# Kernel optimization log

Measured on AMD Instinct MI355X. Metric: run time of the kernel, lower is better.

Reference implementation:

```python
import jax, jax.numpy as jnp
import numpy as np

VALUE_RANGE = 16
D_MODEL = 1024
NUM_TILES = 8
NUM_FREQS = 6
BATCH = 65536
TEMPERATURE = 0.5


def _fourier(x):
    # x: (B,) -> (B, 2*NUM_FREQS); freqs = 2**[0..F)
    freqs = 2.0 ** jnp.arange(NUM_FREQS, dtype=jnp.float32)
    ang = x[:, None] * (2.0 * np.pi / VALUE_RANGE) * freqs[None, :]
    return jnp.concatenate([jnp.sin(ang), jnp.cos(ang)], axis=-1)


def _layernorm(x, g, b, eps=1e-5):
    m = jnp.mean(x, axis=-1, keepdims=True)
    v = jnp.var(x, axis=-1, keepdims=True)
    return (x - m) * jax.lax.rsqrt(v + eps) * g + b


def _gelu(x):
    return jax.nn.gelu(x, approximate=False)  # torch nn.GELU() default is exact erf


def setup_inputs() -> dict:
    key = jax.random.key(0)
    ks = jax.random.split(key, 16)
    d, T, F4 = D_MODEL, NUM_TILES, 4 * NUM_FREQS
    s = lambda i, shape, scale: (jax.random.normal(ks[i], shape, jnp.float32) * scale)
    return {
        "a": jax.random.uniform(ks[0], (BATCH,), jnp.float32, 0.0, float(VALUE_RANGE)),
        "b": jax.random.uniform(ks[1], (BATCH,), jnp.float32, 0.0, float(VALUE_RANGE)),
        "W_in": s(2, (F4, d), 0.05), "b_in": jnp.zeros((d,), jnp.float32),
        "ln_g": jnp.ones((d,), jnp.float32), "ln_b": jnp.zeros((d,), jnp.float32),
        "Wr1_sum": s(3, (d, d), 0.03), "br1_sum": jnp.zeros((d,), jnp.float32),
        "Wr2_sum": s(4, (d, T), 0.03), "br2_sum": jnp.zeros((T,), jnp.float32),
        "Wr1_diff": s(5, (d, d), 0.03), "br1_diff": jnp.zeros((d,), jnp.float32),
        "Wr2_diff": s(6, (d, T), 0.03), "br2_diff": jnp.zeros((T,), jnp.float32),
        "We1": s(7, (T, d, 2 * d), 0.03), "be1": jnp.zeros((T, 2 * d), jnp.float32),
        "We2": s(8, (T, 2 * d, d), 0.02), "be2": jnp.zeros((T, d), jnp.float32),
        "w_sum": s(9, (d,), 0.03), "bs": jnp.zeros((), jnp.float32),
        "w_diff": s(10, (d,), 0.03), "bd": jnp.zeros((), jnp.float32),
    }


def reference(a, b, W_in, b_in, ln_g, ln_b,
              Wr1_sum, br1_sum, Wr2_sum, br2_sum,
              Wr1_diff, br1_diff, Wr2_diff, br2_diff,
              We1, be1, We2, be2, w_sum, bs, w_diff, bd):
    # Shared encoder
    x = jnp.concatenate([_fourier(a), _fourier(b)], axis=-1)      # (B, 4F)
    x = _gelu(_layernorm(x @ W_in + b_in, ln_g, ln_b))            # (B, d)
    # Top-1 routing (temperature scaling does not change argmax, kept for fidelity)
    sum_logits = (_gelu(x @ Wr1_sum + br1_sum) @ Wr2_sum + br2_sum) / TEMPERATURE
    diff_logits = (_gelu(x @ Wr1_diff + br1_diff) @ Wr2_diff + br2_diff) / TEMPERATURE
    sum_tile = jnp.argmax(sum_logits, axis=-1)                    # (B,)
    diff_tile = jnp.argmax(diff_logits, axis=-1)                  # (B,)
    # Expert dispatch: loop over small fixed num_tiles, mask-combine per token.
    sum_hidden = jnp.zeros_like(x)
    diff_hidden = jnp.zeros_like(x)
    for t in range(We1.shape[0]):
        y = _gelu(x @ We1[t] + be1[t]) @ We2[t] + be2[t]          # (B, d)
        sum_hidden = sum_hidden + jnp.where((sum_tile == t)[:, None], y, 0.0)
        diff_hidden = diff_hidden + jnp.where((diff_tile == t)[:, None], y, 0.0)
    sum_pred = sum_hidden @ w_sum + bs                            # (B,)
    diff_pred = diff_hidden @ w_diff + bd                         # (B,)
    return (sum_pred, diff_pred)
```

## Files before the change

kernel.cpp:

```cpp
#include <hip/hip_runtime.h>
#include <math.h>


#define BT 65536
#define D 1024
#define NT 8
#define DH 2048
#define RCAP 8192
#define DELTA 0.025f
#define XJCAP 768

typedef _Float16 f16;
typedef _Float16 f16x8 __attribute__((ext_vector_type(8)));
typedef _Float16 f16x4 __attribute__((ext_vector_type(4)));
typedef float f32x16 __attribute__((ext_vector_type(16)));

__device__ __forceinline__ float gelu_f(float v) {
    return 0.5f * v * (1.0f + erff(v * 0.70710678118654752440f));
}

__device__ __forceinline__ float gelu_fast(float x) {
    float ax = fabsf(x) * 0.70710678118654752440f;
    float t = __builtin_amdgcn_rcpf(1.0f + 0.3275911f * ax);
    float p = t * (0.254829592f + t * (-0.284496736f + t * (1.421413741f +
              t * (-1.453152027f + t * 1.061405429f))));
    float er = 1.0f - p * __expf(-ax * ax);
    er = copysignf(er, x);
    return 0.5f * x * (1.0f + er);
}

__device__ __forceinline__ void gload16(const void* g, void* l) {
    __builtin_amdgcn_global_load_lds(
        (const __attribute__((address_space(1))) void*)g,
        (__attribute__((address_space(3))) void*)l, 16, 0, 0);
}

__global__ __launch_bounds__(256) void k_prev(
    const float* __restrict__ We2, const float* __restrict__ w_sum,
    const float* __restrict__ w_diff, const float* __restrict__ be2,
    const float* __restrict__ bs, const float* __restrict__ bd,
    float* __restrict__ v_sum, float* __restrict__ v_diff,
    float* __restrict__ c_sum, float* __restrict__ c_diff)
{
    int bid = blockIdx.x;
    if (bid < 4096) {
        int row  = bid * 4 + (threadIdx.x >> 6);
        int lane = threadIdx.x & 63;
        const float* r = We2 + (size_t)row * D;
        float s1 = 0.f, s2 = 0.f;
        #pragma unroll
        for (int i = 0; i < 4; i++) {
            int o4 = (lane + 64 * i) * 4;
            float4 w = *(const float4*)(r + o4);
            float4 u = *(const float4*)(w_sum + o4);
            float4 v = *(const float4*)(w_diff + o4);
            s1 += w.x*u.x + w.y*u.y + w.z*u.z + w.w*u.w;
            s2 += w.x*v.x + w.y*v.y + w.z*v.z + w.w*v.w;
        }
        #pragma unroll
        for (int m = 32; m >= 1; m >>= 1) {
            s1 += __shfl_xor(s1, m, 64);
            s2 += __shfl_xor(s2, m, 64);
        }
        if (lane == 0) { v_sum[row] = s1; v_diff[row] = s2; }
    } else {
        int t = threadIdx.x;
        if (t < 8) {
            float s = 0.f; const float* r = be2 + t * D;
            for (int k = 0; k < D; k++) s += r[k] * w_sum[k];
            c_sum[t] = s + bs[0];
        } else if (t < 16) {
            int tt = t - 8;
            float s = 0.f; const float* r = be2 + tt * D;
            for (int k = 0; k < D; k++) s += r[k] * w_diff[k];
            c_diff[tt] = s + bd[0];
        }
    }
}

__global__ __launch_bounds__(256) void k_cvt(
    const float* __restrict__ We1, f16* __restrict__ We1T)
{
    __shared__ float tile[64][65];
    int b = blockIdx.x;
    int e = b >> 9, rem = b & 511;
    int kt = rem >> 5, nt = rem & 31;
    int tid = threadIdx.x;
    const float* src = We1 + ((size_t)e * D + kt * 64) * DH + nt * 64;
    #pragma unroll
    for (int i = 0; i < 16; i++) {
        int idx = tid + 256 * i;
        int kk = idx >> 6, nn = idx & 63;
        tile[kk][nn] = src[(size_t)kk * DH + nn];
    }
    __syncthreads();
    f16* dst = We1T + ((size_t)e * DH + nt * 64) * D + kt * 64;
    #pragma unroll
    for (int i = 0; i < 16; i++) {
        int idx = tid + 256 * i;
        int nn = idx >> 6, kk = idx & 63;
        dst[(size_t)nn * D + kk] = (f16)tile[kk][nn];
    }
}

__global__ __launch_bounds__(256) void k_cvtR(
    const float* __restrict__ Wr1s, const float* __restrict__ Wr1d,
    f16* __restrict__ Wr1Tf)
{
    __shared__ float tile[64][65];
    int b = blockIdx.x;
    int z = b >> 8, rem = b & 255;
    int kt = rem >> 4, nt2 = rem & 15;
    int tid = threadIdx.x;
    const float* W = z ? Wr1d : Wr1s;
    const float* src = W + (size_t)(kt * 64) * 1024 + nt2 * 64;
    #pragma unroll
    for (int i = 0; i < 16; i++) {
        int idx = tid + 256 * i;
        int kk = idx >> 6, nn = idx & 63;
        tile[kk][nn] = src[(size_t)kk * 1024 + nn];
    }
    __syncthreads();
    f16* dst = Wr1Tf + (size_t)(z * 1024 + nt2 * 64) * 1024 + kt * 64;
    #pragma unroll
    for (int i = 0; i < 16; i++) {
        int idx = tid + 256 * i;
        int nn = idx >> 6, kk = idx & 63;
        dst[(size_t)nn * 1024 + kk] = (f16)tile[kk][nn];
    }
}

__global__ __launch_bounds__(256) void k_fuse(
    const float* __restrict__ br1s, const float* __restrict__ br1d,
    const float* __restrict__ Wr2s, const float* __restrict__ Wr2d,
    float* __restrict__ br1f, float* __restrict__ w2f)
{
    int tid = threadIdx.x;
    for (int n = tid; n < 2048; n += 256) {
        br1f[n] = (n < 1024) ? br1s[n] : br1d[n - 1024];
        const float* src = (n < 1024) ? (Wr2s + (size_t)n * 8)
                                      : (Wr2d + (size_t)(n - 1024) * 8);
        #pragma unroll
        for (int o = 0; o < 8; o++) w2f[(size_t)n * 8 + o] = src[o];
    }
}

__global__ __launch_bounds__(256) void k_enc(
    const float* __restrict__ a, const float* __restrict__ b,
    const float* __restrict__ W_in, const float* __restrict__ b_in,
    const float* __restrict__ ln_g, const float* __restrict__ ln_b,
    float* __restrict__ x, f16* __restrict__ xh, int tok0)
{
    __shared__ float x0[64][24];
    __shared__ float red[8];
    int tid = threadIdx.x;
    float4 Wc[24];
    #pragma unroll
    for (int f = 0; f < 24; f++) Wc[f] = *(const float4*)(W_in + f * D + tid * 4);
    float4 bi = *(const float4*)(b_in + tid * 4);
    float4 gg = *(const float4*)(ln_g + tid * 4);
    float4 bb = *(const float4*)(ln_b + tid * 4);
    int base = tok0 + blockIdx.x * 64;

    for (int idx = tid; idx < 64 * 12; idx += 256) {
        int t = idx / 12, q = idx - t * 12;
        int fr = q % 6;
        float in = (q < 6) ? a[base + t] : b[base + t];
        float ang = (in * 0.39269908169872414f) * (float)(1 << fr);
        int off = (q < 6) ? 0 : 12;
        x0[t][off + fr]     = sinf(ang);
        x0[t][off + 6 + fr] = cosf(ang);
    }
    __syncthreads();

    int lane = tid & 63, wid = tid >> 6;
    for (int t = 0; t < 64; t++) {
        float4 p = bi;
        #pragma unroll
        for (int f = 0; f < 24; f++) {
            float xv = x0[t][f];
            p.x += xv * Wc[f].x; p.y += xv * Wc[f].y;
            p.z += xv * Wc[f].z; p.w += xv * Wc[f].w;
        }
        float s1 = p.x + p.y + p.z + p.w;
        float s2 = p.x*p.x + p.y*p.y + p.z*p.z + p.w*p.w;
        #pragma unroll
        for (int m = 32; m >= 1; m >>= 1) {
            s1 += __shfl_xor(s1, m, 64);
            s2 += __shfl_xor(s2, m, 64);
        }
        if (lane == 0) { red[wid] = s1; red[4 + wid] = s2; }
        __syncthreads();
        float mean = (red[0] + red[1] + red[2] + red[3]) * (1.f / 1024.f);
        float ms   = (red[4] + red[5] + red[6] + red[7]) * (1.f / 1024.f);
        float inv  = 1.f / sqrtf(ms - mean * mean + 1e-5f);
        float4 o;
        o.x = gelu_f((p.x - mean) * inv * gg.x + bb.x);
        o.y = gelu_f((p.y - mean) * inv * gg.y + bb.y);
        o.z = gelu_f((p.z - mean) * inv * gg.z + bb.z);
        o.w = gelu_f((p.w - mean) * inv * gg.w + bb.w);
        size_t row = (size_t)(blockIdx.x * 64 + t);
        *(float4*)(x + row * D + tid * 4) = o;
        f16x4 h; h[0] = (f16)o.x; h[1] = (f16)o.y; h[2] = (f16)o.z; h[3] = (f16)o.w;
        *(f16x4*)(xh + row * D + tid * 4) = h;
        __syncthreads();
    }
}

__global__ __launch_bounds__(256, 3) void k_rtrm(
    const f16* __restrict__ xh, const f16* __restrict__ Wr1Tf,
    const float* __restrict__ br1f, const float* __restrict__ w2f,
    float* __restrict__ part)
{
    __shared__ char smem[40960] __attribute__((aligned(16)));
    int bid = blockIdx.x;
    int ntile = bid & 7;
    int ttile = bid >> 3;
    int tid = threadIdx.x;
    int lane = tid & 63, wid = tid >> 6;
    int hi = lane >> 5, l31 = lane & 31;
    int sg = tid >> 3, sc = tid & 7;

    const char* xb = (const char*)xh + (size_t)(ttile * 64) * 2048;
    const char* wb = (const char*)Wr1Tf + (size_t)(ntile * 256) * 2048;
    size_t goff = (size_t)sg * 2048 + (size_t)((sc * 16) ^ ((sg & 7) << 4));

    int axor = (l31 & 7) << 4;
    int kx[4];
    #pragma unroll
    for (int ks = 0; ks < 4; ks++) kx[ks] = (ks * 32 + hi * 16) ^ axor;
    int arow[2], brow[2];
    #pragma unroll
    for (int mi = 0; mi < 2; mi++) arow[mi] = (wid * 64 + mi * 32 + l31) * 128;
    #pragma unroll
    for (int ni = 0; ni < 2; ni++) brow[ni] = 32768 + (ni * 32 + l31) * 128;

    f32x16 acc[2][2];
    #pragma unroll
    for (int mi = 0; mi < 2; mi++)
        #pragma unroll
        for (int ni = 0; ni < 2; ni++) acc[mi][ni] = (f32x16)(0.0f);

    for (int k0 = 0; k0 < 1024; k0 += 64) {
        __syncthreads();
        #pragma unroll
        for (int i = 0; i < 8; i++)
            gload16(wb + (size_t)i * 32 * 2048 + k0 * 2 + goff,
                    smem + i * 4096 + wid * 1024);
        #pragma unroll
        for (int i = 0; i < 2; i++)
            gload16(xb + (size_t)i * 32 * 2048 + k0 * 2 + goff,
                    smem + 32768 + i * 4096 + wid * 1024);
        __syncthreads();
        #pragma unroll
        for (int ks = 0; ks < 4; ks++) {
            f16x8 a0 = *(const f16x8*)(smem + arow[0] + kx[ks]);
            f16x8 a1 = *(const f16x8*)(smem + arow[1] + kx[ks]);
            f16x8 b0 = *(const f16x8*)(smem + brow[0] + kx[ks]);
            f16x8 b1 = *(const f16x8*)(smem + brow[1] + kx[ks]);
            acc[0][0] = __builtin_amdgcn_mfma_f32_32x32x16_f16(a0, b0, acc[0][0], 0, 0, 0);
            acc[0][1] = __builtin_amdgcn_mfma_f32_32x32x16_f16(a0, b1, acc[0][1], 0, 0, 0);
            acc[1][0] = __builtin_amdgcn_mfma_f32_32x32x16_f16(a1, b0, acc[1][0], 0, 0, 0);
            acc[1][1] = __builtin_amdgcn_mfma_f32_32x32x16_f16(a1, b1, acc[1][1], 0, 0, 0);
        }
    }

    float lp[2][8] = {};
    #pragma unroll
    for (int mi = 0; mi < 2; mi++) {
        #pragma unroll
        for (int r = 0; r < 16; r++) {
            int nl = wid * 64 + mi * 32 + (r & 3) + 8 * (r >> 2) + 4 * hi;
            int gn = ntile * 256 + nl;
            float b1 = br1f[gn];
            float4 wa = *(const float4*)(w2f + (size_t)gn * 8);
            float4 wc = *(const float4*)(w2f + (size_t)gn * 8 + 4);
            float h0 = gelu_fast(acc[mi][0][r] + b1);
            float h1 = gelu_fast(acc[mi][1][r] + b1);
            lp[0][0] += h0*wa.x; lp[0][1] += h0*wa.y;
            lp[0][2] += h0*wa.z; lp[0][3] += h0*wa.w;
            lp[0][4] += h0*wc.x; lp[0][5] += h0*wc.y;
            lp[0][6] += h0*wc.z; lp[0][7] += h0*wc.w;
            lp[1][0] += h1*wa.x; lp[1][1] += h1*wa.y;
            lp[1][2] += h1*wa.z; lp[1][3] += h1*wa.w;
            lp[1][4] += h1*wc.x; lp[1][5] += h1*wc.y;
            lp[1][6] += h1*wc.z; lp[1][7] += h1*wc.w;
        }
    }
    #pragma unroll
    for (int ni = 0; ni < 2; ni++)
        #pragma unroll
        for (int o = 0; o < 8; o++)
            lp[ni][o] += __shfl_xor(lp[ni][o], 32, 64);
    __syncthreads();
    float* redf = (float*)smem;
    if (hi == 0) {
        #pragma unroll
        for (int ni = 0; ni < 2; ni++)
            #pragma unroll
            for (int o = 0; o < 8; o++)
                redf[(wid * 64 + ni * 32 + l31) * 8 + o] = lp[ni][o];
    }
    __syncthreads();
    for (int idx = tid; idx < 512; idx += 256) {
        int tok = idx >> 3, o = idx & 7;
        float s = ((redf[(0 * 64 + tok) * 8 + o]  + redf[(1 * 64 + tok) * 8 + o])
                 +  redf[(2 * 64 + tok) * 8 + o]) + redf[(3 * 64 + tok) * 8 + o];
        part[((size_t)(ttile * 64 + tok) * 8 + ntile) * 8 + o] = s;
    }
}

__device__ __forceinline__ void emit_tasks(int tok, int ts, int td,
                                           int* tasks, int* cnts, int tstr)
{
    if (ts == td) {
        int s = atomicAdd(&cnts[ts], 1);
        tasks[ts * tstr + s] = tok | (3 << 17);
    } else {
        int s1 = atomicAdd(&cnts[ts], 1);
        tasks[ts * tstr + s1] = tok | (1 << 17);
        int s2 = atomicAdd(&cnts[td], 1);
        tasks[td * tstr + s2] = tok | (2 << 17);
    }
}

__global__ __launch_bounds__(256) void k_amx2(
    const float* __restrict__ part, const float* __restrict__ b2s,
    const float* __restrict__ b2d, int* __restrict__ tasks,
    int* __restrict__ ctrl, int* __restrict__ redo, int tstr)
{
    int i = blockIdx.x * 256 + threadIdx.x;
    const float* p = part + (size_t)i * 64;
    float Ls[8], Ld[8];
    #pragma unroll
    for (int o = 0; o < 8; o++) { Ls[o] = b2s[o]; Ld[o] = b2d[o]; }
    #pragma unroll
    for (int nt = 0; nt < 4; nt++)
        #pragma unroll
        for (int o = 0; o < 8; o++) Ls[o] += p[nt * 8 + o];
    #pragma unroll
    for (int nt = 4; nt < 8; nt++)
        #pragma unroll
        for (int o = 0; o < 8; o++) Ld[o] += p[nt * 8 + o];

    int as = 0; float m1s = Ls[0];
    #pragma unroll
    for (int o = 1; o < 8; o++) if (Ls[o] > m1s) { m1s = Ls[o]; as = o; }
    float m2s = -1e30f;
    #pragma unroll
    for (int o = 0; o < 8; o++) if (o != as && Ls[o] > m2s) m2s = Ls[o];
    int ad = 0; float m1d = Ld[0];
    #pragma unroll
    for (int o = 1; o < 8; o++) if (Ld[o] > m1d) { m1d = Ld[o]; ad = o; }
    float m2d = -1e30f;
    #pragma unroll
    for (int o = 0; o < 8; o++) if (o != ad && Ld[o] > m2d) m2d = Ld[o];

    if ((m1s - m2s) < DELTA || (m1d - m2d) < DELTA) {
        int s = atomicAdd(&ctrl[8], 1);
        if (s < RCAP) { redo[s] = i; return; }
    }
    emit_tasks(i, as, ad, tasks, ctrl, tstr);
}

__global__ __launch_bounds__(256) void k_redo(
    const float* __restrict__ x,
    const float* __restrict__ Wr1s, const float* __restrict__ br1s,
    const float* __restrict__ Wr2s,
    const float* __restrict__ Wr1d, const float* __restrict__ br1d,
    const float* __restrict__ Wr2d,
    const int* __restrict__ redo, const int* __restrict__ ctrl,
    float* __restrict__ rlogp)
{
    int rcnt = min(ctrl[8], RCAP);
    int nt = blockIdx.y, z = blockIdx.z;
    const float* Wr1 = z ? Wr1d : Wr1s;
    const float* br1 = z ? br1d : br1s;
    const float* Wr2 = z ? Wr2d : Wr2s;
    __shared__ float As[64][72];
    __shared__ float Bs[64][132];
    __shared__ int tokR[64];
    int tid = threadIdx.x;
    int tr = tid >> 5, tc = tid & 31;

    for (int mc = blockIdx.x; mc * 64 < rcnt; mc += gridDim.x) {
        __syncthreads();
        if (tid < 64) tokR[tid] = redo[min(mc * 64 + tid, rcnt - 1)];
        __syncthreads();
        float acc[8][4] = {};
        const float* wb = Wr1 + nt * 128;
        for (int k0 = 0; k0 < D; k0 += 64) {
            __syncthreads();
            {
                int row = tid >> 2, q = tid & 3;
                const float* xr = x + (size_t)tokR[row] * D + k0;
                #pragma unroll
                for (int i = 0; i < 4; i++) {
                    int f4i = q + 4 * i;
                    float4 v = *(const float4*)(xr + f4i * 4);
                    int k = f4i * 4;
                    As[k][row] = v.x; As[k+1][row] = v.y;
                    As[k+2][row] = v.z; As[k+3][row] = v.w;
                }
            }
            {
                #pragma unroll
                for (int i = 0; i < 8; i++) {
                    int idx = tid + 256 * i;
                    int k = idx >> 5, nq = idx & 31;
                    float4 v = *(const float4*)(wb + (size_t)(k0 + k) * D + nq * 4);
                    *(float4*)&Bs[k][nq * 4] = v;
                }
            }
            __syncthreads();
            #pragma unroll 4
            for (int kk = 0; kk < 64; kk++) {
                float4 a0 = *(const float4*)&As[kk][tr * 8];
                float4 a1 = *(const float4*)&As[kk][tr * 8 + 4];
                float4 bv = *(const float4*)&Bs[kk][tc * 4];
                float ar[8] = {a0.x,a0.y,a0.z,a0.w,a1.x,a1.y,a1.z,a1.w};
                #pragma unroll
                for (int i = 0; i < 8; i++) {
                    acc[i][0] += ar[i] * bv.x;
                    acc[i][1] += ar[i] * bv.y;
                    acc[i][2] += ar[i] * bv.z;
                    acc[i][3] += ar[i] * bv.w;
                }
            }
        }
        float lp[8][8] = {};
        #pragma unroll
        for (int j = 0; j < 4; j++) {
            int col = nt * 128 + tc * 4 + j;
            float b1 = br1[col];
            float w2[8];
            #pragma unroll
            for (int o = 0; o < 8; o++) w2[o] = Wr2[col * 8 + o];
            #pragma unroll
            for (int i = 0; i < 8; i++) {
                float h = gelu_f(acc[i][j] + b1);
                #pragma unroll
                for (int o = 0; o < 8; o++) lp[i][o] += h * w2[o];
            }
        }
        #pragma unroll
        for (int m = 16; m >= 1; m >>= 1) {
            #pragma unroll
            for (int i = 0; i < 8; i++)
                #pragma unroll
                for (int o = 0; o < 8; o++)
                    lp[i][o] += __shfl_xor(lp[i][o], m, 64);
        }
        if (tc == 0) {
            #pragma unroll
            for (int i = 0; i < 8; i++) {
                int slot = mc * 64 + tr * 8 + i;
                if (slot < rcnt) {
                    float* p = rlogp + ((size_t)slot * 8 + nt) * 16 + z * 8;
                    #pragma unroll
                    for (int o = 0; o < 8; o++) p[o] = lp[i][o];
                }
            }
        }
    }
}

__global__ __launch_bounds__(256) void k_amx3(
    const float* __restrict__ rlogp, const int* __restrict__ redo,
    const float* __restrict__ b2s, const float* __restrict__ b2d,
    int* __restrict__ tasks, int* __restrict__ ctrl, int tstr)
{
    int rcnt = min(ctrl[8], RCAP);
    for (int s = blockIdx.x * 256 + threadIdx.x; s < rcnt; s += gridDim.x * 256) {
        int tok = redo[s];
        float L[16] = {};
        for (int nt = 0; nt < 8; nt++) {
            const float* p = rlogp + ((size_t)s * 8 + nt) * 16;
            #pragma unroll
            for (int o = 0; o < 16; o++) L[o] += p[o];
        }
        float Ls[8], Ld[8];
        #pragma unroll
        for (int o = 0; o < 8; o++) { Ls[o] = L[o] + b2s[o]; Ld[o] = L[8 + o] + b2d[o]; }
        int ts = 0; float bv = Ls[0];
        #pragma unroll
        for (int o = 1; o < 8; o++) if (Ls[o] > bv) { bv = Ls[o]; ts = o; }
        int td = 0; bv = Ld[0];
        #pragma unroll
        for (int o = 1; o < 8; o++) if (Ld[o] > bv) { bv = Ld[o]; td = o; }
        emit_tasks(tok, ts, td, tasks, ctrl, tstr);
    }
}

__global__ void k_sched(const int* __restrict__ ctrl, int* __restrict__ xjob)
{
    __shared__ int seg[17];
    __shared__ int Jt[2];
    int tid = threadIdx.x;
    if (tid == 0) {
        int o = 0;
        for (int e = 0; e < 8; e++) {
            int nt2 = (ctrl[e] + 63) >> 6;
            seg[e * 2]     = o; o += nt2;
            seg[e * 2 + 1] = o; o += nt2;
        }
        seg[16] = o;
        Jt[0] = o; Jt[1] = (o + 7) >> 3;
    }
    __syncthreads();
    int J = Jt[0], target = Jt[1];
    for (int g = tid; g < J; g += blockDim.x) {
        int s = 0;
        while (s < 15 && seg[s + 1] <= g) s++;
        int e = s >> 1, ch = s & 1, rt = g - seg[s];
        int x = g / target; if (x > 7) x = 7;
        int pos = g - x * target;
        xjob[x * XJCAP + pos] = e | (ch << 3) | (rt << 4);
    }
    if (tid < 8) {
        int c = J - tid * target;
        if (c < 0) c = 0;
        if (c > target) c = target;
        xjob[8 * XJCAP + tid] = c;
    }
}

__global__ __launch_bounds__(256, 3) void k_expm(
    const f16* __restrict__ xh, const f16* __restrict__ We1T,
    const float* __restrict__ be1, const float* __restrict__ v_sum,
    const float* __restrict__ v_diff, const float* __restrict__ c_sum,
    const float* __restrict__ c_diff, const int* __restrict__ tasks,
    const int* __restrict__ counts, const int* __restrict__ xjob,
    float* __restrict__ ppS, float* __restrict__ ppD, int qn)
{
    int xcd  = blockIdx.x & 7;
    int slot = blockIdx.x >> 3;
    int nj = xjob[8 * XJCAP + xcd];
    int tstr = 2 * qn;

    __shared__ char smem[40960] __attribute__((aligned(16)));
    __shared__ int tokL[64];
    __shared__ int flgL[64];
    __shared__ float redS[2][64];
    __shared__ float redD[2][64];

    int tid = threadIdx.x;
    int lane = tid & 63;
    int wid  = tid >> 6;
    int wr = wid >> 1, wc = wid & 1;
    int hi = lane >> 5, l31 = lane & 31;
    int sg = tid >> 3, sc = tid & 7;
    size_t goffc = (size_t)((sc * 16) ^ ((sg & 7) << 4));
    size_t b_off = (size_t)sg * 2048 + goffc;

    const char* xh_b = (const char*)xh;

    int axor = (l31 & 7) << 4;
    int kx[4];
    #pragma unroll
    for (int ks = 0; ks < 4; ks++) kx[ks] = (ks * 32 + hi * 16) ^ axor;
    int arow = (wr * 32 + l31) * 128;
    int nrow[4];
    #pragma unroll
    for (int ni = 0; ni < 4; ni++) nrow[ni] = 8192 + (wc * 128 + ni * 32 + l31) * 128;

    for (int j = slot; j < nj; j += 256) {
        int jv = xjob[xcd * XJCAP + j];
        int e  = jv & 7;
        int ch = (jv >> 3) & 1;
        int rt = jv >> 4;
        int cnt = counts[e];
        int r0 = rt * 64;
        const char* we1t_e = (const char*)(We1T + (size_t)e * DH * D);

        __syncthreads();
        if (tid < 64) {
            int idx = r0 + tid;
            int tv = tasks[e * tstr + min(idx, cnt - 1)];
            tokL[tid] = tv & 0xFFFF;
            flgL[tid] = (idx < cnt) ? ((tv >> 17) & 3) : 0;
        }
        __syncthreads();
        size_t asrc[2];
        #pragma unroll
        for (int i = 0; i < 2; i++)
            asrc[i] = (size_t)tokL[i * 32 + sg] * 2048 + goffc;

        float ss[16] = {}, sd[16] = {};

        for (int n0 = ch * 1024; n0 < ch * 1024 + 1024; n0 += 256) {
            f32x16 acc[4];
            #pragma unroll
            for (int ni = 0; ni < 4; ni++) acc[ni] = (f32x16)(0.0f);
            const char* bsrc = we1t_e + (size_t)n0 * 2048 + b_off;

            for (int k0 = 0; k0 < D; k0 += 64) {
                __syncthreads();
                gload16(xh_b + asrc[0] + k0 * 2, smem + wid * 1024);
                gload16(xh_b + asrc[1] + k0 * 2, smem + 4096 + wid * 1024);
                #pragma unroll
                for (int i = 0; i < 8; i++)
                    gload16(bsrc + (size_t)i * 32 * 2048 + k0 * 2,
                            smem + 8192 + i * 4096 + wid * 1024);
                __syncthreads();
                #pragma unroll
                for (int ks = 0; ks < 4; ks++) {
                    f16x8 av = *(const f16x8*)(smem + arow + kx[ks]);
                    #pragma unroll
                    for (int ni = 0; ni < 4; ni++) {
                        f16x8 bf = *(const f16x8*)(smem + nrow[ni] + kx[ks]);
                        acc[ni] = __builtin_amdgcn_mfma_f32_32x32x16_f16(av, bf, acc[ni], 0, 0, 0);
                    }
                }
            }
            #pragma unroll
            for (int ni = 0; ni < 4; ni++) {
                int col = n0 + wc * 128 + ni * 32 + l31;
                float b1 = be1[e * DH + col];
                float vs = v_sum[(size_t)e * DH + col];
                float vd = v_diff[(size_t)e * DH + col];
                #pragma unroll
                for (int r = 0; r < 16; r++) {
                    float h = gelu_fast(acc[ni][r] + b1);
                    ss[r] += h * vs;
                    sd[r] += h * vd;
                }
            }
        }

        #pragma unroll
        for (int m = 16; m >= 1; m >>= 1) {
            #pragma unroll
            for (int r = 0; r < 16; r++) {
                ss[r] += __shfl_xor(ss[r], m, 64);
                sd[r] += __shfl_xor(sd[r], m, 64);
            }
        }
        if (l31 == 0) {
            #pragma unroll
            for (int r = 0; r < 16; r++) {
                int row = wr * 32 + (r & 3) + 8 * (r >> 2) + 4 * hi;
                redS[wc][row] = ss[r];
                redD[wc][row] = sd[r];
            }
        }
        __syncthreads();
        if (tid < 64) {
            int idx = r0 + tid;
            if (idx < cnt) {
                int fl = flgL[tid];
                int tok = tokL[tid];
                float s = redS[0][tid] + redS[1][tid];
                float d = redD[0][tid] + redD[1][tid];
                if (ch == 0) { s += c_sum[e]; d += c_diff[e]; }
                if (fl & 1) ppS[ch * qn + tok] = s;
                if (fl & 2) ppD[ch * qn + tok] = d;
            }
        }
    }
}

__global__ __launch_bounds__(256) void k_fin(
    const float* __restrict__ ppS, const float* __restrict__ ppD,
    float* __restrict__ out, int tok0, int qn)
{
    int i = blockIdx.x * 256 + threadIdx.x;
    out[tok0 + i]      = ppS[i] + ppS[qn + i];
    out[BT + tok0 + i] = ppD[i] + ppD[qn + i];
}

extern "C" void kernel_launch(void* const* d_in, const int* in_sizes, int n_in,
                              void* d_out, int out_size, void* d_ws, size_t ws_size,
                              hipStream_t stream)
{
    const float* a      = (const float*)d_in[0];
    const float* b      = (const float*)d_in[1];
    const float* W_in   = (const float*)d_in[2];
    const float* b_in   = (const float*)d_in[3];
    const float* ln_g   = (const float*)d_in[4];
    const float* ln_b   = (const float*)d_in[5];
    const float* Wr1s   = (const float*)d_in[6];
    const float* br1s   = (const float*)d_in[7];
    const float* Wr2s   = (const float*)d_in[8];
    const float* br2s   = (const float*)d_in[9];
    const float* Wr1d   = (const float*)d_in[10];
    const float* br1d   = (const float*)d_in[11];
    const float* Wr2d   = (const float*)d_in[12];
    const float* br2d   = (const float*)d_in[13];
    const float* We1    = (const float*)d_in[14];
    const float* be1    = (const float*)d_in[15];
    const float* We2    = (const float*)d_in[16];
    const float* be2    = (const float*)d_in[17];
    const float* w_sum  = (const float*)d_in[18];
    const float* bs     = (const float*)d_in[19];
    const float* w_diff = (const float*)d_in[20];
    const float* bd     = (const float*)d_in[21];
    float* out = (float*)d_out;

    auto plan = [&](size_t qn) -> size_t {
        size_t o = 0;
        auto al = [&](size_t bytes) { o = (o + bytes + 255) & ~(size_t)255; };
        al((size_t)NT * DH * 4); al((size_t)NT * DH * 4); al(64); al(64);
        al(qn * D * 4); al(qn * D * 2); al(qn * 64 * 4);
        al((size_t)RCAP * 128 * 4); al(qn * 4); al((size_t)NT * 2 * qn * 4);
        al(64); al((size_t)(8 * XJCAP + 8) * 4);
        al(2 * qn * 4); al(2 * qn * 4);
        al((size_t)NT * DH * D * 2); al((size_t)2048 * 1024 * 2);
        al(2048 * 4); al(2048 * 8 * 4);
        return o;
    };
    int qn = 65536;
    while (qn > 16384 && plan((size_t)qn) > ws_size) qn >>= 1;
    if (plan((size_t)qn) > ws_size) {
        hipMemsetAsync(d_out, 0, (size_t)out_size * 4, stream);
        return;
    }
    int npass = BT / qn;
    int tstr = 2 * qn;

    char* w = (char*)d_ws;
    size_t off = 0;
    auto alloc = [&](size_t bytes) -> char* {
        char* p = w + off;
        off = (off + bytes + 255) & ~(size_t)255;
        return p;
    };
    float* v_sum   = (float*)alloc((size_t)NT * DH * 4);
    float* v_diff  = (float*)alloc((size_t)NT * DH * 4);
    float* c_sum   = (float*)alloc(64);
    float* c_diff  = (float*)alloc(64);
    float* x       = (float*)alloc((size_t)qn * D * 4);
    f16*   xh      = (f16*)alloc((size_t)qn * D * 2);
    float* part    = (float*)alloc((size_t)qn * 64 * 4);
    float* rlogp   = (float*)alloc((size_t)RCAP * 128 * 4);
    int*   redo    = (int*)alloc((size_t)qn * 4);
    int*   tasks   = (int*)alloc((size_t)NT * 2 * qn * 4);
    int*   ctrl    = (int*)alloc(64);
    int*   xjob    = (int*)alloc((size_t)(8 * XJCAP + 8) * 4);
    float* ppS     = (float*)alloc((size_t)2 * qn * 4);
    float* ppD     = (float*)alloc((size_t)2 * qn * 4);
    f16*   We1T    = (f16*)alloc((size_t)NT * DH * D * 2);
    f16*   Wr1Tf   = (f16*)alloc((size_t)2048 * 1024 * 2);
    float* br1f    = (float*)alloc((size_t)2048 * 4);
    float* w2f     = (float*)alloc((size_t)2048 * 8 * 4);

    k_cvt <<<dim3(4096), dim3(256), 0, stream>>>(We1, We1T);
    k_cvtR<<<dim3(512),  dim3(256), 0, stream>>>(Wr1s, Wr1d, Wr1Tf);
    k_fuse<<<dim3(1),    dim3(256), 0, stream>>>(br1s, br1d, Wr2s, Wr2d, br1f, w2f);
    k_prev<<<dim3(4097), dim3(256), 0, stream>>>(We2, w_sum, w_diff, be2, bs, bd,
                                                 v_sum, v_diff, c_sum, c_diff);
    for (int q = 0; q < npass; q++) {
        int tok0 = q * qn;
        k_enc<<<dim3(qn / 64), dim3(256), 0, stream>>>(a, b, W_in, b_in, ln_g, ln_b, x, xh, tok0);
        k_rtrm<<<dim3(qn / 64 * 8), dim3(256), 0, stream>>>(xh, Wr1Tf, br1f, w2f, part);
        hipMemsetAsync(ctrl, 0, 64, stream);
        k_amx2<<<dim3(qn / 256), dim3(256), 0, stream>>>(part, br2s, br2d, tasks, ctrl, redo, tstr);
        k_redo<<<dim3(64, 8, 2), dim3(256), 0, stream>>>(x, Wr1s, br1s, Wr2s, Wr1d, br1d, Wr2d,
                                                         redo, ctrl, rlogp);
        k_amx3<<<dim3(16), dim3(256), 0, stream>>>(rlogp, redo, br2s, br2d, tasks, ctrl, tstr);
        k_sched<<<dim3(1), dim3(256), 0, stream>>>(ctrl, xjob);
        k_expm<<<dim3(2048), dim3(256), 0, stream>>>(xh, We1T, be1, v_sum, v_diff,
                                                     c_sum, c_diff, tasks, ctrl, xjob,
                                                     ppS, ppD, qn);
        k_fin<<<dim3(qn / 256), dim3(256), 0, stream>>>(ppS, ppD, out, tok0, qn);
    }
}
```

Before: 2.902 ms.

## Split sum/diff router redo lists, shrink margin, enlarge expert tile to 128 rows

```diff
diff --git a/kernel.cpp b/kernel.cpp
--- a/kernel.cpp
+++ b/kernel.cpp
@@ -7,7 +7,7 @@
 #define NT 8
 #define DH 2048
 #define RCAP 8192
-#define DELTA 0.025f
+#define DELTA 0.010f
 #define XJCAP 768
 
 typedef _Float16 f16;
@@ -327,7 +327,8 @@
 __global__ __launch_bounds__(256) void k_amx2(
     const float* __restrict__ part, const float* __restrict__ b2s,
     const float* __restrict__ b2d, int* __restrict__ tasks,
-    int* __restrict__ ctrl, int* __restrict__ redo, int tstr)
+    int* __restrict__ ctrl, int* __restrict__ redoS, int* __restrict__ redoD,
+    int tstr)
 {
     int i = blockIdx.x * 256 + threadIdx.x;
     const float* p = part + (size_t)i * 64;
@@ -356,11 +357,15 @@
     #pragma unroll
     for (int o = 0; o < 8; o++) if (o != ad && Ld[o] > m2d) m2d = Ld[o];
 
-    if ((m1s - m2s) < DELTA || (m1d - m2d) < DELTA) {
-        int s = atomicAdd(&ctrl[8], 1);
-        if (s < RCAP) { redo[s] = i; return; }
-    }
-    emit_tasks(i, as, ad, tasks, ctrl, tstr);
+    bool sM = (m1s - m2s) < DELTA;
+    bool dM = (m1d - m2d) < DELTA;
+    if (!sM && !dM) { emit_tasks(i, as, ad, tasks, ctrl, tstr); return; }
+    int posS = -1, posD = -1;
+    if (sM) { posS = atomicAdd(&ctrl[8], 1); if (posS >= RCAP) { sM = false; posS = -1; } }
+    if (dM) { posD = atomicAdd(&ctrl[9], 1); if (posD >= RCAP) { dM = false; posD = -1; } }
+    if (!sM && !dM) { emit_tasks(i, as, ad, tasks, ctrl, tstr); return; }
+    if (sM) redoS[posS] = i | (ad << 17) | ((dM ? 1 : 0) << 20);
+    if (dM) redoD[posD] = i | (as << 17) | ((sM ? 1 : 0) << 20);
 }
 
 __global__ __launch_bounds__(256) void k_redo(
@@ -369,14 +374,17 @@
     const float* __restrict__ Wr2s,
     const float* __restrict__ Wr1d, const float* __restrict__ br1d,
     const float* __restrict__ Wr2d,
-    const int* __restrict__ redo, const int* __restrict__ ctrl,
-    float* __restrict__ rlogp)
-{
-    int rcnt = min(ctrl[8], RCAP);
+    const int* __restrict__ redoS, const int* __restrict__ redoD,
+    const int* __restrict__ ctrl,
+    float* __restrict__ rlogpS, float* __restrict__ rlogpD)
+{
     int nt = blockIdx.y, z = blockIdx.z;
+    int rcnt = min(ctrl[8 + z], RCAP);
     const float* Wr1 = z ? Wr1d : Wr1s;
     const float* br1 = z ? br1d : br1s;
     const float* Wr2 = z ? Wr2d : Wr2s;
+    const int* list = z ? redoD : redoS;
+    float* rlogp = z ? rlogpD : rlogpS;
     __shared__ float As[64][72];
     __shared__ float Bs[64][132];
     __shared__ int tokR[64];
@@ -385,7 +393,7 @@
 
     for (int mc = blockIdx.x; mc * 64 < rcnt; mc += gridDim.x) {
         __syncthreads();
-        if (tid < 64) tokR[tid] = redo[min(mc * 64 + tid, rcnt - 1)];
+        if (tid < 64) tokR[tid] = list[min(mc * 64 + tid, rcnt - 1)] & 0xFFFF;
         __syncthreads();
         float acc[8][4] = {};
         const float* wb = Wr1 + nt * 128;
@@ -456,7 +464,7 @@
             for (int i = 0; i < 8; i++) {
                 int slot = mc * 64 + tr * 8 + i;
                 if (slot < rcnt) {
-                    float* p = rlogp + ((size_t)slot * 8 + nt) * 16 + z * 8;
+                    float* p = rlogp + (size_t)slot * 64 + nt * 8;
                     #pragma unroll
                     for (int o = 0; o < 8; o++) p[o] = lp[i][o];
                 }
@@ -465,29 +473,53 @@
     }
 }
 
-__global__ __launch_bounds__(256) void k_amx3(
-    const float* __restrict__ rlogp, const int* __restrict__ redo,
-    const float* __restrict__ b2s, const float* __restrict__ b2d,
-    int* __restrict__ tasks, int* __restrict__ ctrl, int tstr)
+__global__ __launch_bounds__(256) void k_amx3d(
+    const float* __restrict__ rlogpD, const int* __restrict__ redoD,
+    const float* __restrict__ b2d, int* __restrict__ tasks,
+    int* __restrict__ ctrl, int* __restrict__ adx, int tstr)
+{
+    int rcnt = min(ctrl[9], RCAP);
+    for (int s = blockIdx.x * 256 + threadIdx.x; s < rcnt; s += gridDim.x * 256) {
+        int entry = redoD[s];
+        int tok = entry & 0xFFFF;
+        float L[8] = {};
+        for (int nt = 0; nt < 8; nt++) {
+            const float* p = rlogpD + (size_t)s * 64 + nt * 8;
+            #pragma unroll
+            for (int o = 0; o < 8; o++) L[o] += p[o];
+        }
+        #pragma unroll
+        for (int o = 0; o < 8; o++) L[o] += b2d[o];
+        int td = 0; float bv = L[0];
+        #pragma unroll
+        for (int o = 1; o < 8; o++) if (L[o] > bv) { bv = L[o]; td = o; }
+        adx[tok] = td;
+        if (!((entry >> 20) & 1))
+            emit_tasks(tok, (entry >> 17) & 7, td, tasks, ctrl, tstr);
+    }
+}
+
+__global__ __launch_bounds__(256) void k_amx3s(
+    const float* __restrict__ rlogpS, const int* __restrict__ redoS,
+    const float* __restrict__ b2s, int* __restrict__ tasks,
+    int* __restrict__ ctrl, const int* __restrict__ adx, int tstr)
 {
     int rcnt = min(ctrl[8], RCAP);
     for (int s = blockIdx.x * 256 + threadIdx.x; s < rcnt; s += gridDim.x * 256) {
-        int tok = redo[s];
-        float L[16] = {};
+        int entry = redoS[s];
+        int tok = entry & 0xFFFF;
+        float L[8] = {};
         for (int nt = 0; nt < 8; nt++) {
-            const float* p = rlogp + ((size_t)s * 8 + nt) * 16;
-            #pragma unroll
-            for (int o = 0; o < 16; o++) L[o] += p[o];
-        }
-        float Ls[8], Ld[8];
-        #pragma unroll
-        for (int o = 0; o < 8; o++) { Ls[o] = L[o] + b2s[o]; Ld[o] = L[8 + o] + b2d[o]; }
-        int ts = 0; float bv = Ls[0];
-        #pragma unroll
-        for (int o = 1; o < 8; o++) if (Ls[o] > bv) { bv = Ls[o]; ts = o; }
-        int td = 0; bv = Ld[0];
-        #pragma unroll
-        for (int o = 1; o < 8; o++) if (Ld[o] > bv) { bv = Ld[o]; td = o; }
+            const float* p = rlogpS + (size_t)s * 64 + nt * 8;
+            #pragma unroll
+            for (int o = 0; o < 8; o++) L[o] += p[o];
+        }
+        #pragma unroll
+        for (int o = 0; o < 8; o++) L[o] += b2s[o];
+        int ts = 0; float bv = L[0];
+        #pragma unroll
+        for (int o = 1; o < 8; o++) if (L[o] > bv) { bv = L[o]; ts = o; }
+        int td = ((entry >> 20) & 1) ? adx[tok] : ((entry >> 17) & 7);
         emit_tasks(tok, ts, td, tasks, ctrl, tstr);
     }
 }
@@ -500,7 +532,7 @@
     if (tid == 0) {
         int o = 0;
         for (int e = 0; e < 8; e++) {
-            int nt2 = (ctrl[e] + 63) >> 6;
+            int nt2 = (ctrl[e] + 127) >> 7;
             seg[e * 2]     = o; o += nt2;
             seg[e * 2 + 1] = o; o += nt2;
         }
@@ -525,7 +557,7 @@
     }
 }
 
-__global__ __launch_bounds__(256, 3) void k_expm(
+__global__ __launch_bounds__(256) void k_expm(
     const f16* __restrict__ xh, const f16* __restrict__ We1T,
     const float* __restrict__ be1, const float* __restrict__ v_sum,
     const float* __restrict__ v_diff, const float* __restrict__ c_sum,
@@ -538,11 +570,11 @@
     int nj = xjob[8 * XJCAP + xcd];
     int tstr = 2 * qn;
 
-    __shared__ char smem[40960] __attribute__((aligned(16)));
-    __shared__ int tokL[64];
-    __shared__ int flgL[64];
-    __shared__ float redS[2][64];
-    __shared__ float redD[2][64];
+    __shared__ char smem[49152] __attribute__((aligned(16)));
+    __shared__ int tokL[128];
+    __shared__ int flgL[128];
+    __shared__ float redS[2][128];
+    __shared__ float redD[2][128];
 
     int tid = threadIdx.x;
     int lane = tid & 63;
@@ -550,8 +582,7 @@
     int wr = wid >> 1, wc = wid & 1;
     int hi = lane >> 5, l31 = lane & 31;
     int sg = tid >> 3, sc = tid & 7;
-    size_t goffc = (size_t)((sc * 16) ^ ((sg & 7) << 4));
-    size_t b_off = (size_t)sg * 2048 + goffc;
+    int stoff = sg * 128 + ((sc * 16) ^ ((sg & 7) << 4));
 
     const char* xh_b = (const char*)xh;
 
@@ -559,10 +590,11 @@
     int kx[4];
     #pragma unroll
     for (int ks = 0; ks < 4; ks++) kx[ks] = (ks * 32 + hi * 16) ^ axor;
-    int arow = (wr * 32 + l31) * 128;
-    int nrow[4];
-    #pragma unroll
-    for (int ni = 0; ni < 4; ni++) nrow[ni] = 8192 + (wc * 128 + ni * 32 + l31) * 128;
+    int arow[2], nrow[4];
+    #pragma unroll
+    for (int mi = 0; mi < 2; mi++) arow[mi] = (wr * 64 + mi * 32 + l31) * 128;
+    #pragma unroll
+    for (int ni = 0; ni < 4; ni++) nrow[ni] = 16384 + (wc * 128 + ni * 32 + l31) * 128;
 
     for (int j = slot; j < nj; j += 256) {
         int jv = xjob[xcd * XJCAP + j];
@@ -570,46 +602,57 @@
         int ch = (jv >> 3) & 1;
         int rt = jv >> 4;
         int cnt = counts[e];
-        int r0 = rt * 64;
+        int r0 = rt * 128;
         const char* we1t_e = (const char*)(We1T + (size_t)e * DH * D);
+        size_t bs_off = (size_t)sg * (D * 2) + sc * 16;
 
         __syncthreads();
-        if (tid < 64) {
+        if (tid < 128) {
             int idx = r0 + tid;
             int tv = tasks[e * tstr + min(idx, cnt - 1)];
             tokL[tid] = tv & 0xFFFF;
             flgL[tid] = (idx < cnt) ? ((tv >> 17) & 3) : 0;
         }
         __syncthreads();
-        size_t asrc[2];
-        #pragma unroll
-        for (int i = 0; i < 2; i++)
-            asrc[i] = (size_t)tokL[i * 32 + sg] * 2048 + goffc;
-
-        float ss[16] = {}, sd[16] = {};
+        size_t asrc_off[4];
+        #pragma unroll
+        for (int i = 0; i < 4; i++)
+            asrc_off[i] = (size_t)tokL[i * 32 + sg] * (D * 2) + sc * 16;
+
+        float ss[2][16] = {}, sd[2][16] = {};
 
         for (int n0 = ch * 1024; n0 < ch * 1024 + 1024; n0 += 256) {
-            f32x16 acc[4];
-            #pragma unroll
-            for (int ni = 0; ni < 4; ni++) acc[ni] = (f32x16)(0.0f);
-            const char* bsrc = we1t_e + (size_t)n0 * 2048 + b_off;
+            f32x16 acc[2][4];
+            #pragma unroll
+            for (int mi = 0; mi < 2; mi++)
+                #pragma unroll
+                for (int ni = 0; ni < 4; ni++)
+                    acc[mi][ni] = (f32x16)(0.0f);
+
+            const char* bsrc0 = we1t_e + (size_t)n0 * (D * 2) + bs_off;
 
             for (int k0 = 0; k0 < D; k0 += 64) {
                 __syncthreads();
-                gload16(xh_b + asrc[0] + k0 * 2, smem + wid * 1024);
-                gload16(xh_b + asrc[1] + k0 * 2, smem + 4096 + wid * 1024);
-                #pragma unroll
-                for (int i = 0; i < 8; i++)
-                    gload16(bsrc + (size_t)i * 32 * 2048 + k0 * 2,
-                            smem + 8192 + i * 4096 + wid * 1024);
+                #pragma unroll
+                for (int i = 0; i < 4; i++) {
+                    int4 v = *(const int4*)(xh_b + asrc_off[i] + k0 * 2);
+                    *(int4*)(smem + i * 4096 + stoff) = v;
+                }
+                #pragma unroll
+                for (int i = 0; i < 8; i++) {
+                    int4 v = *(const int4*)(bsrc0 + (size_t)i * 32 * (D * 2) + k0 * 2);
+                    *(int4*)(smem + 16384 + i * 4096 + stoff) = v;
+                }
                 __syncthreads();
                 #pragma unroll
                 for (int ks = 0; ks < 4; ks++) {
-                    f16x8 av = *(const f16x8*)(smem + arow + kx[ks]);
+                    f16x8 a0 = *(const f16x8*)(smem + arow[0] + kx[ks]);
+                    f16x8 a1 = *(const f16x8*)(smem + arow[1] + kx[ks]);
                     #pragma unroll
                     for (int ni = 0; ni < 4; ni++) {
                         f16x8 bf = *(const f16x8*)(smem + nrow[ni] + kx[ks]);
-                        acc[ni] = __builtin_amdgcn_mfma_f32_32x32x16_f16(av, bf, acc[ni], 0, 0, 0);
+                        acc[0][ni] = __builtin_amdgcn_mfma_f32_32x32x16_f16(a0, bf, acc[0][ni], 0, 0, 0);
+                        acc[1][ni] = __builtin_amdgcn_mfma_f32_32x32x16_f16(a1, bf, acc[1][ni], 0, 0, 0);
                     }
                 }
             }
@@ -620,32 +663,39 @@
                 float vs = v_sum[(size_t)e * DH + col];
                 float vd = v_diff[(size_t)e * DH + col];
                 #pragma unroll
+                for (int mi = 0; mi < 2; mi++) {
+                    #pragma unroll
+                    for (int r = 0; r < 16; r++) {
+                        float h = gelu_fast(acc[mi][ni][r] + b1);
+                        ss[mi][r] += h * vs;
+                        sd[mi][r] += h * vd;
+                    }
+                }
+            }
+        }
+
+        #pragma unroll
+        for (int m = 16; m >= 1; m >>= 1) {
+            #pragma unroll
+            for (int mi = 0; mi < 2; mi++)
+                #pragma unroll
                 for (int r = 0; r < 16; r++) {
-                    float h = gelu_fast(acc[ni][r] + b1);
-                    ss[r] += h * vs;
-                    sd[r] += h * vd;
-                }
-            }
-        }
-
-        #pragma unroll
-        for (int m = 16; m >= 1; m >>= 1) {
-            #pragma unroll
-            for (int r = 0; r < 16; r++) {
-                ss[r] += __shfl_xor(ss[r], m, 64);
-                sd[r] += __shfl_xor(sd[r], m, 64);
-            }
+                    ss[mi][r] += __shfl_xor(ss[mi][r], m, 64);
+                    sd[mi][r] += __shfl_xor(sd[mi][r], m, 64);
+                }
         }
         if (l31 == 0) {
             #pragma unroll
-            for (int r = 0; r < 16; r++) {
-                int row = wr * 32 + (r & 3) + 8 * (r >> 2) + 4 * hi;
-                redS[wc][row] = ss[r];
-                redD[wc][row] = sd[r];
-            }
+            for (int mi = 0; mi < 2; mi++)
+                #pragma unroll
+                for (int r = 0; r < 16; r++) {
+                    int row = wr * 64 + mi * 32 + (r & 3) + 8 * (r >> 2) + 4 * hi;
+                    redS[wc][row] = ss[mi][r];
+                    redD[wc][row] = sd[mi][r];
+                }
         }
         __syncthreads();
-        if (tid < 64) {
+        if (tid < 128) {
             int idx = r0 + tid;
             if (idx < cnt) {
                 int fl = flgL[tid];
@@ -702,7 +752,9 @@
         auto al = [&](size_t bytes) { o = (o + bytes + 255) & ~(size_t)255; };
         al((size_t)NT * DH * 4); al((size_t)NT * DH * 4); al(64); al(64);
         al(qn * D * 4); al(qn * D * 2); al(qn * 64 * 4);
-        al((size_t)RCAP * 128 * 4); al(qn * 4); al((size_t)NT * 2 * qn * 4);
+        al((size_t)RCAP * 64 * 4); al((size_t)RCAP * 64 * 4);
+        al((size_t)RCAP * 4); al((size_t)RCAP * 4); al(qn * 4);
+        al((size_t)NT * 2 * qn * 4);
         al(64); al((size_t)(8 * XJCAP + 8) * 4);
         al(2 * qn * 4); al(2 * qn * 4);
         al((size_t)NT * DH * D * 2); al((size_t)2048 * 1024 * 2);
@@ -732,8 +784,11 @@
     float* x       = (float*)alloc((size_t)qn * D * 4);
     f16*   xh      = (f16*)alloc((size_t)qn * D * 2);
     float* part    = (float*)alloc((size_t)qn * 64 * 4);
-    float* rlogp   = (float*)alloc((size_t)RCAP * 128 * 4);
-    int*   redo    = (int*)alloc((size_t)qn * 4);
+    float* rlogpS  = (float*)alloc((size_t)RCAP * 64 * 4);
+    float* rlogpD  = (float*)alloc((size_t)RCAP * 64 * 4);
+    int*   redoS   = (int*)alloc((size_t)RCAP * 4);
+    int*   redoD   = (int*)alloc((size_t)RCAP * 4);
+    int*   adx     = (int*)alloc((size_t)qn * 4);
     int*   tasks   = (int*)alloc((size_t)NT * 2 * qn * 4);
     int*   ctrl    = (int*)alloc(64);
     int*   xjob    = (int*)alloc((size_t)(8 * XJCAP + 8) * 4);
@@ -754,10 +809,12 @@
         k_enc<<<dim3(qn / 64), dim3(256), 0, stream>>>(a, b, W_in, b_in, ln_g, ln_b, x, xh, tok0);
         k_rtrm<<<dim3(qn / 64 * 8), dim3(256), 0, stream>>>(xh, Wr1Tf, br1f, w2f, part);
         hipMemsetAsync(ctrl, 0, 64, stream);
-        k_amx2<<<dim3(qn / 256), dim3(256), 0, stream>>>(part, br2s, br2d, tasks, ctrl, redo, tstr);
-        k_redo<<<dim3(64, 8, 2), dim3(256), 0, stream>>>(x, Wr1s, br1s, Wr2s, Wr1d, br1d, Wr2d,
-                                                         redo, ctrl, rlogp);
-        k_amx3<<<dim3(16), dim3(256), 0, stream>>>(rlogp, redo, br2s, br2d, tasks, ctrl, tstr);
+        k_amx2<<<dim3(qn / 256), dim3(256), 0, stream>>>(part, br2s, br2d, tasks, ctrl,
+                                                         redoS, redoD, tstr);
+        k_redo<<<dim3(32, 8, 2), dim3(256), 0, stream>>>(x, Wr1s, br1s, Wr2s, Wr1d, br1d, Wr2d,
+                                                         redoS, redoD, ctrl, rlogpS, rlogpD);
+        k_amx3d<<<dim3(16), dim3(256), 0, stream>>>(rlogpD, redoD, br2d, tasks, ctrl, adx, tstr);
+        k_amx3s<<<dim3(16), dim3(256), 0, stream>>>(rlogpS, redoS, br2s, tasks, ctrl, adx, tstr);
         k_sched<<<dim3(1), dim3(256), 0, stream>>>(ctrl, xjob);
         k_expm<<<dim3(2048), dim3(256), 0, stream>>>(xh, We1T, be1, v_sum, v_diff,
                                                      c_sum, c_diff, tasks, ctrl, xjob,
```

After: 2.474 ms. 1.17x faster.
